# Kernel tuning notes

Measured on AMD Instinct MI355X. Metric: run time of the kernel, lower is better.

The kernel has to match this reference:

```python
import jax, jax.numpy as jnp
import numpy as np

E, K, D = 50000, 8, 256
NH = 4
HD = D // NH
SCALE = HD ** -0.5
EPS = 1e-8


def setup_inputs() -> dict:
    key = jax.random.key(0)
    ks = jax.random.split(key, 16)
    p = lambda k, shp: (jax.random.normal(k, shp, dtype=jnp.float32) * 0.02)
    return {
        "x_i": jax.random.normal(ks[0], (E, D), dtype=jnp.float32),
        "x_j": jax.random.normal(ks[1], (E, D), dtype=jnp.float32),
        "h_seq_i": jax.random.normal(ks[2], (E, K, D), dtype=jnp.float32),
        "h_seq_j": jax.random.normal(ks[3], (E, K, D), dtype=jnp.float32),
        "edge_emb": jax.random.normal(ks[4], (E, D), dtype=jnp.float32),
        "Wq": p(ks[5], (D, D)), "bq": jnp.zeros((D,), jnp.float32),
        "Wk": p(ks[6], (D, D)), "bk": jnp.zeros((D,), jnp.float32),
        "We1": p(ks[7], (D, D // 2)), "be1": jnp.zeros((D // 2,), jnp.float32),
        "We2": p(ks[8], (D // 2, 1)), "be2": jnp.zeros((1,), jnp.float32),
        "Wo1": p(ks[9], (3, 16)), "bo1": jnp.zeros((16,), jnp.float32),
        "Wo2": p(ks[10], (16, 1)), "bo2": jnp.zeros((1,), jnp.float32),
    }


def reference(x_i, x_j, h_seq_i, h_seq_j, edge_emb,
              Wq, bq, Wk, bk, We1, be1, We2, be2, Wo1, bo1, Wo2, bo2):
    # (A) attribute alignment: cosine similarity mapped to (0,1)
    num = jnp.sum(x_i * x_j, axis=-1)
    den = jnp.maximum(jnp.linalg.norm(x_i, axis=-1), EPS) * \
          jnp.maximum(jnp.linalg.norm(x_j, axis=-1), EPS)
    attr_score = (num / den + 1.0) / 2.0  # [E]

    # (B) activity alignment: tiny cross-attention, mean of softmax diagonal
    Q = (jnp.einsum('ekd,df->ekf', h_seq_i, Wq) + bq).reshape(E, K, NH, HD)
    Kv = (jnp.einsum('ekd,df->ekf', h_seq_j, Wk) + bk).reshape(E, K, NH, HD)
    scores = jnp.einsum('eqhd,ekhd->ehqk', Q, Kv) * SCALE  # [E,NH,K,K]
    attn = jax.nn.softmax(scores, axis=-1)
    diag = jnp.diagonal(attn, axis1=-2, axis2=-1)  # [E,NH,K]
    activity_score = diag.mean(axis=(-1, -2))  # [E]

    # (C) edge plausibility MLP (exact GELU as in torch default)
    h = jax.nn.gelu(edge_emb @ We1 + be1, approximate=False)
    edge_score = jax.nn.sigmoid((h @ We2 + be2)[..., 0])  # [E]

    signals = jnp.stack([attr_score, activity_score, edge_score], axis=-1)  # [E,3]
    out = jax.nn.gelu(signals @ Wo1 + bo1, approximate=False) @ Wo2 + bo2
    return jax.nn.sigmoid(out[..., 0])  # [E]
```

## Files before the change

### kernel.cpp

```cpp
#include <hip/hip_runtime.h>

#define E_TOT   50000
#define DD      256
#define KSEQ    8
#define NHEAD   4
#define HDIM    64
#define TE      4
#define SCALE_V 0.125f

typedef __attribute__((ext_vector_type(4))) float f32x4;
typedef __attribute__((ext_vector_type(8))) short short8;

__device__ __forceinline__ unsigned short f2bf(float f) {
    unsigned u = __float_as_uint(f);
    u += 0x7fffu + ((u >> 16) & 1u);
    return (unsigned short)(u >> 16);
}
__device__ __forceinline__ float bf2f(unsigned short h) {
    return __uint_as_float(((unsigned)h) << 16);
}
__device__ __forceinline__ float gelu_exact(float x) {
    return 0.5f * x * (1.0f + erff(x * 0.70710678118654752440f));
}
__device__ __forceinline__ float sigmoidf(float x) {
    return 1.0f / (1.0f + __expf(-x));
}

__global__ void prep_weights(const float* __restrict__ Wq,
                             const float* __restrict__ Wk,
                             const float* __restrict__ We1,
                             unsigned short* __restrict__ wqT,
                             unsigned short* __restrict__ wkT,
                             unsigned short* __restrict__ wb1) {
    int i = blockIdx.x * 256 + threadIdx.x;
    if (i < 131072) {
        int which = i >> 16;
        int j = i & 65535;
        int k = j >> 8, n = j & 255;
        const float* W = which ? Wk : Wq;
        unsigned short* o = which ? wkT : wqT;
        o[n * 256 + k] = f2bf(W[j]);
    } else {
        int j = i - 131072;
        wb1[j] = f2bf(We1[j]);
    }
}

__global__ void score_attr_edge(const float* __restrict__ x_i,
                                const float* __restrict__ x_j,
                                const float* __restrict__ emb,
                                const unsigned short* __restrict__ wb1,
                                const float* __restrict__ be1,
                                const float* __restrict__ We2,
                                const float* __restrict__ be2,
                                float* __restrict__ attr_out,
                                float* __restrict__ edge_out) {
    __shared__ float sEmb[4][DD];
    const int wv = threadIdx.x >> 6;
    const int l  = threadIdx.x & 63;
    const int e  = blockIdx.x * 4 + wv;

    f32x4 a = *(const f32x4*)(x_i + (size_t)e * DD + l * 4);
    f32x4 b = *(const f32x4*)(x_j + (size_t)e * DD + l * 4);
    f32x4 ev = *(const f32x4*)(emb + (size_t)e * DD + l * 4);
    float dot = a[0]*b[0] + a[1]*b[1] + a[2]*b[2] + a[3]*b[3];
    float ni  = a[0]*a[0] + a[1]*a[1] + a[2]*a[2] + a[3]*a[3];
    float nj  = b[0]*b[0] + b[1]*b[1] + b[2]*b[2] + b[3]*b[3];
    #pragma unroll
    for (int off = 1; off < 64; off <<= 1) {
        dot += __shfl_xor(dot, off);
        ni  += __shfl_xor(ni,  off);
        nj  += __shfl_xor(nj,  off);
    }
    float na = fmaxf(sqrtf(ni), 1e-8f);
    float nb = fmaxf(sqrtf(nj), 1e-8f);
    if (l == 0) attr_out[e] = (dot / (na * nb) + 1.0f) * 0.5f;

    sEmb[wv][l*4+0] = ev[0]; sEmb[wv][l*4+1] = ev[1];
    sEmb[wv][l*4+2] = ev[2]; sEmb[wv][l*4+3] = ev[3];
    __syncthreads();

    float acc0 = 0.f, acc1 = 0.f;
    #pragma unroll 8
    for (int k = 0; k < DD; ++k) {
        float ek = sEmb[wv][k];
        unsigned u = *(const unsigned*)(wb1 + k * 128 + 2 * l);
        acc0 = fmaf(ek, bf2f((unsigned short)(u & 0xffffu)), acc0);
        acc1 = fmaf(ek, bf2f((unsigned short)(u >> 16)),     acc1);
    }
    float h0 = gelu_exact(acc0 + be1[2 * l]);
    float h1 = gelu_exact(acc1 + be1[2 * l + 1]);
    float s  = h0 * We2[2 * l] + h1 * We2[2 * l + 1];
    #pragma unroll
    for (int off = 1; off < 64; off <<= 1) s += __shfl_xor(s, off);
    if (l == 0) edge_out[e] = sigmoidf(s + be2[0]);
}

__device__ __forceinline__ void do_gemm(const unsigned short (*A)[DD + 8],
                                        const unsigned short* __restrict__ Wt,
                                        f32x4 acc[2][4], int l, int w) {
    const int lr = l & 15, lq = l >> 4;
    #pragma unroll
    for (int ks = 0; ks < 8; ++ks) {
        const short8 a0 = *(const short8*)&A[lr][ks * 32 + lq * 8];
        const short8 a1 = *(const short8*)&A[16 + lr][ks * 32 + lq * 8];
        #pragma unroll
        for (int n = 0; n < 4; ++n) {
            const int col = (w * 4 + n) * 16 + lr;
            const short8 bv = *(const short8*)(Wt + col * 256 + ks * 32 + lq * 8);
            acc[0][n] = __builtin_amdgcn_mfma_f32_16x16x32_bf16(a0, bv, acc[0][n], 0, 0, 0);
            acc[1][n] = __builtin_amdgcn_mfma_f32_16x16x32_bf16(a1, bv, acc[1][n], 0, 0, 0);
        }
    }
}

__device__ __forceinline__ void writeback(unsigned short (*A)[DD + 8],
                                          const f32x4 acc[2][4],
                                          const float* __restrict__ bias,
                                          int l, int w) {
    const int lr = l & 15, lq = l >> 4;
    #pragma unroll
    for (int n = 0; n < 4; ++n) {
        const int col = (w * 4 + n) * 16 + lr;
        const float bs = bias[col];
        #pragma unroll
        for (int m = 0; m < 2; ++m) {
            #pragma unroll
            for (int v = 0; v < 4; ++v) {
                const int row = m * 16 + lq * 4 + v;
                A[row][col] = f2bf(acc[m][n][v] + bs);
            }
        }
    }
}

__global__ __launch_bounds__(256, 4)
void fused_attn(const float* __restrict__ h_i,
                const float* __restrict__ h_j,
                const unsigned short* __restrict__ wqT,
                const unsigned short* __restrict__ wkT,
                const float* __restrict__ bq,
                const float* __restrict__ bk,
                const float* __restrict__ Wo1,
                const float* __restrict__ bo1,
                const float* __restrict__ Wo2,
                const float* __restrict__ bo2,
                const float* __restrict__ attr_ws,
                const float* __restrict__ edge_ws,
                float* __restrict__ out) {
    __shared__ unsigned short Abf[2][TE * KSEQ][DD + 8];
    __shared__ float actLds[TE];

    const int t = threadIdx.x;
    const int w = t >> 6;
    const int l = t & 63;
    const size_t base = (size_t)blockIdx.x * (TE * KSEQ * DD);

    f32x4 stg[16];
    #pragma unroll
    for (int i = 0; i < 16; ++i) {
        const int f  = i * 256 + t;
        const float* src = (f >> 11) ? h_j : h_i;
        stg[i] = *(const f32x4*)(src + base + (size_t)(f & 2047) * 4);
    }
    #pragma unroll
    for (int i = 0; i < 16; ++i) {
        const int f  = i * 256 + t;
        const int T  = f >> 11;
        const int ff = f & 2047;
        ushort4 u = make_ushort4(f2bf(stg[i][0]), f2bf(stg[i][1]),
                                 f2bf(stg[i][2]), f2bf(stg[i][3]));
        *(ushort4*)&Abf[T][ff >> 6][(ff & 63) * 4] = u;
    }
    __syncthreads();

    {
        f32x4 acc[2][4] = {};
        do_gemm(Abf[0], wqT, acc, l, w);
        __syncthreads();
        writeback(Abf[0], acc, bq, l, w);
    }
    {
        f32x4 acc[2][4] = {};
        do_gemm(Abf[1], wkT, acc, l, w);
        __syncthreads();
        writeback(Abf[1], acc, bk, l, w);
    }
    __syncthreads();

    if (t < 128) {
        const int e = t >> 5, h = (t >> 3) & 3, q = t & 7;
        float qv[64];
        #pragma unroll
        for (int c = 0; c < 8; ++c) {
            short8 v = *(const short8*)&Abf[0][e * 8 + q][h * 64 + c * 8];
            #pragma unroll
            for (int j = 0; j < 8; ++j) qv[c * 8 + j] = bf2f((unsigned short)v[j]);
        }
        float sc[8];
        #pragma unroll
        for (int k = 0; k < 8; ++k) {
            float d = 0.f;
            #pragma unroll
            for (int c = 0; c < 8; ++c) {
                short8 kv = *(const short8*)&Abf[1][e * 8 + k][h * 64 + c * 8];
                #pragma unroll
                for (int j = 0; j < 8; ++j) d = fmaf(qv[c * 8 + j], bf2f((unsigned short)kv[j]), d);
            }
            sc[k] = d * SCALE_V;
        }
        float mx = sc[0];
        #pragma unroll
        for (int k = 1; k < 8; ++k) mx = fmaxf(mx, sc[k]);
        float sum = 0.f, pd = 0.f;
        #pragma unroll
        for (int k = 0; k < 8; ++k) {
            float p = __expf(sc[k] - mx);
            sum += p;
            if (k == q) pd = p;
        }
        float dg = pd / sum;
        #pragma unroll
        for (int off = 1; off < 32; off <<= 1) dg += __shfl_xor(dg, off);
        if ((t & 31) == 0) actLds[e] = dg * (1.0f / 32.0f);
    }
    __syncthreads();

    if (t < TE) {
        const int ge = blockIdx.x * TE + t;
        const float s0 = attr_ws[ge];
        const float s1 = actLds[t];
        const float s2 = edge_ws[ge];
        float acc = bo2[0];
        #pragma unroll
        for (int j = 0; j < 16; ++j) {
            float z = s0 * Wo1[j] + s1 * Wo1[16 + j] + s2 * Wo1[32 + j] + bo1[j];
            acc += gelu_exact(z) * Wo2[j];
        }
        out[ge] = sigmoidf(acc);
    }
}

extern "C" void kernel_launch(void* const* d_in, const int* in_sizes, int n_in,
                              void* d_out, int out_size, void* d_ws, size_t ws_size,
                              hipStream_t stream) {
    const float* x_i  = (const float*)d_in[0];
    const float* x_j  = (const float*)d_in[1];
    const float* h_i  = (const float*)d_in[2];
    const float* h_j  = (const float*)d_in[3];
    const float* emb  = (const float*)d_in[4];
    const float* Wq   = (const float*)d_in[5];
    const float* bq   = (const float*)d_in[6];
    const float* Wk   = (const float*)d_in[7];
    const float* bk   = (const float*)d_in[8];
    const float* We1  = (const float*)d_in[9];
    const float* be1  = (const float*)d_in[10];
    const float* We2  = (const float*)d_in[11];
    const float* be2  = (const float*)d_in[12];
    const float* Wo1  = (const float*)d_in[13];
    const float* bo1  = (const float*)d_in[14];
    const float* Wo2  = (const float*)d_in[15];
    const float* bo2  = (const float*)d_in[16];
    float* out = (float*)d_out;

    unsigned short* wqT = (unsigned short*)d_ws;
    unsigned short* wkT = wqT + 65536;
    unsigned short* wb1 = wkT + 65536;
    float* attr_ws = (float*)((char*)d_ws + 327680);
    float* edge_ws = attr_ws + E_TOT;

    prep_weights<<<640, 256, 0, stream>>>(Wq, Wk, We1, wqT, wkT, wb1);
    score_attr_edge<<<E_TOT / 4, 256, 0, stream>>>(x_i, x_j, emb, wb1, be1, We2, be2,
                                                   attr_ws, edge_ws);
    fused_attn<<<E_TOT / TE, 256, 0, stream>>>(h_i, h_j, wqT, wkT, bq, bk,
                                               Wo1, bo1, Wo2, bo2,
                                               attr_ws, edge_ws, out);
}
```

Baseline: 569.8 us.

## Fuse all score paths into one kernel with LDS DMA and MFMA attention

Merges the attribute/edge scoring kernel into the attention kernel, so one kernel computes cosine, edge MLP, attention and the output MLP without workspace round-trips. h rows are staged through global_load_lds DMA into LDS, with h_j loads overlapped with the Q projection. The edge MLP and the Q·K score computation now use bf16 MFMA instead of scalar FMA loops. LDS use grows and occupancy drops to 3 blocks per CU, and the emb input is rounded to bf16, which changes precision.

```diff
diff --git a/kernel.cpp b/kernel.cpp
--- a/kernel.cpp
+++ b/kernel.cpp
@@ -2,10 +2,8 @@
 
 #define E_TOT   50000
 #define DD      256
-#define KSEQ    8
-#define NHEAD   4
-#define HDIM    64
 #define TE      4
+#define NGROUP  (E_TOT / TE)
 #define SCALE_V 0.125f
 
 typedef __attribute__((ext_vector_type(4))) float f32x4;
@@ -16,14 +14,18 @@
     u += 0x7fffu + ((u >> 16) & 1u);
     return (unsigned short)(u >> 16);
 }
-__device__ __forceinline__ float bf2f(unsigned short h) {
-    return __uint_as_float(((unsigned)h) << 16);
-}
 __device__ __forceinline__ float gelu_exact(float x) {
     return 0.5f * x * (1.0f + erff(x * 0.70710678118654752440f));
 }
 __device__ __forceinline__ float sigmoidf(float x) {
     return 1.0f / (1.0f + __expf(-x));
+}
+
+__device__ __forceinline__ void dma_row16(const float* gbase, float* lds) {
+    const int lane = threadIdx.x & 63;
+    auto gp = (const __attribute__((address_space(1))) char*)(gbase) + lane * 16;
+    auto lp = (__attribute__((address_space(3))) char*)(lds);
+    __builtin_amdgcn_global_load_lds(gp, lp, 16, 0, 0);
 }
 
 __global__ void prep_weights(const float* __restrict__ Wq,
@@ -31,94 +33,43 @@
                              const float* __restrict__ We1,
                              unsigned short* __restrict__ wqT,
                              unsigned short* __restrict__ wkT,
-                             unsigned short* __restrict__ wb1) {
+                             unsigned short* __restrict__ w1T) {
     int i = blockIdx.x * 256 + threadIdx.x;
-    if (i < 131072) {
-        int which = i >> 16;
-        int j = i & 65535;
+    if (i < 65536) {
+        int k = i >> 8, n = i & 255;
+        wqT[n * 256 + k] = f2bf(Wq[i]);
+    } else if (i < 131072) {
+        int j = i - 65536;
         int k = j >> 8, n = j & 255;
-        const float* W = which ? Wk : Wq;
-        unsigned short* o = which ? wkT : wqT;
-        o[n * 256 + k] = f2bf(W[j]);
+        wkT[n * 256 + k] = f2bf(Wk[j]);
     } else {
         int j = i - 131072;
-        wb1[j] = f2bf(We1[j]);
-    }
-}
-
-__global__ void score_attr_edge(const float* __restrict__ x_i,
-                                const float* __restrict__ x_j,
-                                const float* __restrict__ emb,
-                                const unsigned short* __restrict__ wb1,
-                                const float* __restrict__ be1,
-                                const float* __restrict__ We2,
-                                const float* __restrict__ be2,
-                                float* __restrict__ attr_out,
-                                float* __restrict__ edge_out) {
-    __shared__ float sEmb[4][DD];
-    const int wv = threadIdx.x >> 6;
-    const int l  = threadIdx.x & 63;
-    const int e  = blockIdx.x * 4 + wv;
-
-    f32x4 a = *(const f32x4*)(x_i + (size_t)e * DD + l * 4);
-    f32x4 b = *(const f32x4*)(x_j + (size_t)e * DD + l * 4);
-    f32x4 ev = *(const f32x4*)(emb + (size_t)e * DD + l * 4);
-    float dot = a[0]*b[0] + a[1]*b[1] + a[2]*b[2] + a[3]*b[3];
-    float ni  = a[0]*a[0] + a[1]*a[1] + a[2]*a[2] + a[3]*a[3];
-    float nj  = b[0]*b[0] + b[1]*b[1] + b[2]*b[2] + b[3]*b[3];
-    #pragma unroll
-    for (int off = 1; off < 64; off <<= 1) {
-        dot += __shfl_xor(dot, off);
-        ni  += __shfl_xor(ni,  off);
-        nj  += __shfl_xor(nj,  off);
-    }
-    float na = fmaxf(sqrtf(ni), 1e-8f);
-    float nb = fmaxf(sqrtf(nj), 1e-8f);
-    if (l == 0) attr_out[e] = (dot / (na * nb) + 1.0f) * 0.5f;
-
-    sEmb[wv][l*4+0] = ev[0]; sEmb[wv][l*4+1] = ev[1];
-    sEmb[wv][l*4+2] = ev[2]; sEmb[wv][l*4+3] = ev[3];
-    __syncthreads();
-
-    float acc0 = 0.f, acc1 = 0.f;
-    #pragma unroll 8
-    for (int k = 0; k < DD; ++k) {
-        float ek = sEmb[wv][k];
-        unsigned u = *(const unsigned*)(wb1 + k * 128 + 2 * l);
-        acc0 = fmaf(ek, bf2f((unsigned short)(u & 0xffffu)), acc0);
-        acc1 = fmaf(ek, bf2f((unsigned short)(u >> 16)),     acc1);
-    }
-    float h0 = gelu_exact(acc0 + be1[2 * l]);
-    float h1 = gelu_exact(acc1 + be1[2 * l + 1]);
-    float s  = h0 * We2[2 * l] + h1 * We2[2 * l + 1];
-    #pragma unroll
-    for (int off = 1; off < 64; off <<= 1) s += __shfl_xor(s, off);
-    if (l == 0) edge_out[e] = sigmoidf(s + be2[0]);
-}
-
-__device__ __forceinline__ void do_gemm(const unsigned short (*A)[DD + 8],
-                                        const unsigned short* __restrict__ Wt,
-                                        f32x4 acc[2][4], int l, int w) {
-    const int lr = l & 15, lq = l >> 4;
+        int k = j >> 7, n = j & 127;
+        w1T[n * 256 + k] = f2bf(We1[j]);
+    }
+}
+
+__device__ __forceinline__ void proj_gemm(const unsigned short (*A)[260],
+                                          const unsigned short* __restrict__ Wt,
+                                          f32x4 acc[2][4], int lr, int lq, int w) {
     #pragma unroll
     for (int ks = 0; ks < 8; ++ks) {
-        const short8 a0 = *(const short8*)&A[lr][ks * 32 + lq * 8];
-        const short8 a1 = *(const short8*)&A[16 + lr][ks * 32 + lq * 8];
+        short8 a0 = *(const short8*)&A[lr][ks * 32 + lq * 8];
+        short8 a1 = *(const short8*)&A[16 + lr][ks * 32 + lq * 8];
         #pragma unroll
         for (int n = 0; n < 4; ++n) {
             const int col = (w * 4 + n) * 16 + lr;
-            const short8 bv = *(const short8*)(Wt + col * 256 + ks * 32 + lq * 8);
+            short8 bv = *(const short8*)(Wt + col * 256 + ks * 32 + lq * 8);
             acc[0][n] = __builtin_amdgcn_mfma_f32_16x16x32_bf16(a0, bv, acc[0][n], 0, 0, 0);
             acc[1][n] = __builtin_amdgcn_mfma_f32_16x16x32_bf16(a1, bv, acc[1][n], 0, 0, 0);
         }
     }
 }
 
-__device__ __forceinline__ void writeback(unsigned short (*A)[DD + 8],
+__device__ __forceinline__ void writeback(unsigned short (*T)[260],
                                           const f32x4 acc[2][4],
                                           const float* __restrict__ bias,
-                                          int l, int w) {
-    const int lr = l & 15, lq = l >> 4;
+                                          int lr, int lq, int w) {
     #pragma unroll
     for (int n = 0; n < 4; ++n) {
         const int col = (w * 4 + n) * 16 + lr;
@@ -128,117 +79,191 @@
             #pragma unroll
             for (int v = 0; v < 4; ++v) {
                 const int row = m * 16 + lq * 4 + v;
-                A[row][col] = f2bf(acc[m][n][v] + bs);
+                T[row][col] = f2bf(acc[m][n][v] + bs);
             }
         }
     }
 }
 
-__global__ __launch_bounds__(256, 4)
-void fused_attn(const float* __restrict__ h_i,
-                const float* __restrict__ h_j,
-                const unsigned short* __restrict__ wqT,
-                const unsigned short* __restrict__ wkT,
-                const float* __restrict__ bq,
-                const float* __restrict__ bk,
-                const float* __restrict__ Wo1,
-                const float* __restrict__ bo1,
-                const float* __restrict__ Wo2,
-                const float* __restrict__ bo2,
-                const float* __restrict__ attr_ws,
-                const float* __restrict__ edge_ws,
-                float* __restrict__ out) {
-    __shared__ unsigned short Abf[2][TE * KSEQ][DD + 8];
-    __shared__ float actLds[TE];
-
-    const int t = threadIdx.x;
-    const int w = t >> 6;
-    const int l = t & 63;
-    const size_t base = (size_t)blockIdx.x * (TE * KSEQ * DD);
-
-    f32x4 stg[16];
-    #pragma unroll
-    for (int i = 0; i < 16; ++i) {
-        const int f  = i * 256 + t;
-        const float* src = (f >> 11) ? h_j : h_i;
-        stg[i] = *(const f32x4*)(src + base + (size_t)(f & 2047) * 4);
-    }
-    #pragma unroll
-    for (int i = 0; i < 16; ++i) {
-        const int f  = i * 256 + t;
-        const int T  = f >> 11;
-        const int ff = f & 2047;
-        ushort4 u = make_ushort4(f2bf(stg[i][0]), f2bf(stg[i][1]),
-                                 f2bf(stg[i][2]), f2bf(stg[i][3]));
-        *(ushort4*)&Abf[T][ff >> 6][(ff & 63) * 4] = u;
-    }
-    __syncthreads();
-
+__global__ __launch_bounds__(256, 3)
+void fused_all(const float* __restrict__ x_i,
+               const float* __restrict__ x_j,
+               const float* __restrict__ h_i,
+               const float* __restrict__ h_j,
+               const float* __restrict__ emb,
+               const unsigned short* __restrict__ wqT,
+               const unsigned short* __restrict__ wkT,
+               const unsigned short* __restrict__ w1T,
+               const float* __restrict__ bq,
+               const float* __restrict__ bk,
+               const float* __restrict__ be1,
+               const float* __restrict__ We2,
+               const float* __restrict__ be2,
+               const float* __restrict__ Wo1,
+               const float* __restrict__ bo1,
+               const float* __restrict__ Wo2,
+               const float* __restrict__ bo2,
+               float* __restrict__ out) {
+    __shared__ __align__(16) unsigned char ldsA[33280];
+    __shared__ __align__(16) unsigned char ldsH[16640];
+    __shared__ float sEdgeP[4][4];
+
+    float* bufA32 = (float*)ldsA;
+    unsigned short (*bufHI)[260] = (unsigned short (*)[260])ldsH;
+    unsigned short (*tQ)[260]    = (unsigned short (*)[260])ldsA;
+    unsigned short (*tK)[260]    = (unsigned short (*)[260])(ldsA + 16640);
+
+    const int t  = threadIdx.x;
+    const int w  = t >> 6;
+    const int l  = t & 63;
+    const int lr = l & 15, lq = l >> 4;
+    const int g  = blockIdx.x;
+    const size_t rowbase = (size_t)g * 32;
+
+    #pragma unroll
+    for (int rr = 0; rr < 8; ++rr) {
+        const int r = w * 8 + rr;
+        dma_row16(h_i + (rowbase + r) * DD, bufA32 + r * DD);
+    }
+    const int e = g * TE + w;
+    float attr;
     {
-        f32x4 acc[2][4] = {};
-        do_gemm(Abf[0], wqT, acc, l, w);
-        __syncthreads();
-        writeback(Abf[0], acc, bq, l, w);
-    }
+        f32x4 a = *(const f32x4*)(x_i + (size_t)e * DD + l * 4);
+        f32x4 b = *(const f32x4*)(x_j + (size_t)e * DD + l * 4);
+        float dot = a[0]*b[0] + a[1]*b[1] + a[2]*b[2] + a[3]*b[3];
+        float ni  = a[0]*a[0] + a[1]*a[1] + a[2]*a[2] + a[3]*a[3];
+        float nj  = b[0]*b[0] + b[1]*b[1] + b[2]*b[2] + b[3]*b[3];
+        #pragma unroll
+        for (int off = 1; off < 64; off <<= 1) {
+            dot += __shfl_xor(dot, off);
+            ni  += __shfl_xor(ni,  off);
+            nj  += __shfl_xor(nj,  off);
+        }
+        attr = (dot / (fmaxf(sqrtf(ni), 1e-8f) * fmaxf(sqrtf(nj), 1e-8f)) + 1.0f) * 0.5f;
+    }
+    __syncthreads();
+
+    f32x4 stg[8];
+    #pragma unroll
+    for (int i = 0; i < 8; ++i) stg[i] = *(const f32x4*)(bufA32 + (i * 256 + t) * 4);
+    __syncthreads();
+
+    #pragma unroll
+    for (int rr = 0; rr < 8; ++rr) {
+        const int r = w * 8 + rr;
+        dma_row16(h_j + (rowbase + r) * DD, bufA32 + r * DD);
+    }
+    #pragma unroll
+    for (int i = 0; i < 8; ++i) {
+        const int f = i * 256 + t, r = f >> 6, u = f & 63;
+        *(ushort4*)&bufHI[r][u * 4] = make_ushort4(f2bf(stg[i][0]), f2bf(stg[i][1]),
+                                                   f2bf(stg[i][2]), f2bf(stg[i][3]));
+    }
+    __syncthreads();
+
+    f32x4 accQ[2][4] = {};
+    proj_gemm(bufHI, wqT, accQ, lr, lq, w);
+    f32x4 accE[2] = {};
     {
-        f32x4 acc[2][4] = {};
-        do_gemm(Abf[1], wkT, acc, l, w);
-        __syncthreads();
-        writeback(Abf[1], acc, bk, l, w);
-    }
-    __syncthreads();
-
-    if (t < 128) {
-        const int e = t >> 5, h = (t >> 3) & 3, q = t & 7;
-        float qv[64];
-        #pragma unroll
-        for (int c = 0; c < 8; ++c) {
-            short8 v = *(const short8*)&Abf[0][e * 8 + q][h * 64 + c * 8];
+        const float* embrow = emb + ((size_t)g * TE + (lr & 3)) * DD;
+        #pragma unroll
+        for (int ks = 0; ks < 8; ++ks) {
+            f32x4 e0 = *(const f32x4*)(embrow + ks * 32 + lq * 8);
+            f32x4 e1 = *(const f32x4*)(embrow + ks * 32 + lq * 8 + 4);
+            short8 ae;
+            ae[0] = (short)f2bf(e0[0]); ae[1] = (short)f2bf(e0[1]);
+            ae[2] = (short)f2bf(e0[2]); ae[3] = (short)f2bf(e0[3]);
+            ae[4] = (short)f2bf(e1[0]); ae[5] = (short)f2bf(e1[1]);
+            ae[6] = (short)f2bf(e1[2]); ae[7] = (short)f2bf(e1[3]);
             #pragma unroll
-            for (int j = 0; j < 8; ++j) qv[c * 8 + j] = bf2f((unsigned short)v[j]);
-        }
-        float sc[8];
-        #pragma unroll
-        for (int k = 0; k < 8; ++k) {
-            float d = 0.f;
+            for (int n = 0; n < 2; ++n) {
+                const int col = w * 32 + n * 16 + lr;
+                short8 bv = *(const short8*)(w1T + col * 256 + ks * 32 + lq * 8);
+                accE[n] = __builtin_amdgcn_mfma_f32_16x16x32_bf16(ae, bv, accE[n], 0, 0, 0);
+            }
+        }
+    }
+    #pragma unroll
+    for (int i = 0; i < 8; ++i) stg[i] = *(const f32x4*)(bufA32 + (i * 256 + t) * 4);
+    __syncthreads();
+
+    #pragma unroll
+    for (int i = 0; i < 8; ++i) {
+        const int f = i * 256 + t, r = f >> 6, u = f & 63;
+        *(ushort4*)&bufHI[r][u * 4] = make_ushort4(f2bf(stg[i][0]), f2bf(stg[i][1]),
+                                                   f2bf(stg[i][2]), f2bf(stg[i][3]));
+    }
+    writeback(tQ, accQ, bq, lr, lq, w);
+    __syncthreads();
+
+    f32x4 accK[2][4] = {};
+    proj_gemm(bufHI, wkT, accK, lr, lq, w);
+    __syncthreads();
+
+    writeback(tK, accK, bk, lr, lq, w);
+    {
+        float p[4] = {0.f, 0.f, 0.f, 0.f};
+        #pragma unroll
+        for (int n = 0; n < 2; ++n) {
+            const int col = w * 32 + n * 16 + lr;
+            const float b1 = be1[col], w2 = We2[col];
             #pragma unroll
-            for (int c = 0; c < 8; ++c) {
-                short8 kv = *(const short8*)&Abf[1][e * 8 + k][h * 64 + c * 8];
-                #pragma unroll
-                for (int j = 0; j < 8; ++j) d = fmaf(qv[c * 8 + j], bf2f((unsigned short)kv[j]), d);
-            }
-            sc[k] = d * SCALE_V;
-        }
-        float mx = sc[0];
-        #pragma unroll
-        for (int k = 1; k < 8; ++k) mx = fmaxf(mx, sc[k]);
-        float sum = 0.f, pd = 0.f;
-        #pragma unroll
-        for (int k = 0; k < 8; ++k) {
-            float p = __expf(sc[k] - mx);
-            sum += p;
-            if (k == q) pd = p;
-        }
-        float dg = pd / sum;
-        #pragma unroll
-        for (int off = 1; off < 32; off <<= 1) dg += __shfl_xor(dg, off);
-        if ((t & 31) == 0) actLds[e] = dg * (1.0f / 32.0f);
-    }
-    __syncthreads();
-
-    if (t < TE) {
-        const int ge = blockIdx.x * TE + t;
-        const float s0 = attr_ws[ge];
-        const float s1 = actLds[t];
-        const float s2 = edge_ws[ge];
-        float acc = bo2[0];
-        #pragma unroll
-        for (int j = 0; j < 16; ++j) {
-            float z = s0 * Wo1[j] + s1 * Wo1[16 + j] + s2 * Wo1[32 + j] + bo1[j];
-            acc += gelu_exact(z) * Wo2[j];
-        }
-        out[ge] = sigmoidf(acc);
-    }
+            for (int v = 0; v < 4; ++v)
+                p[v] += gelu_exact(accE[n][v] + b1) * w2;
+        }
+        #pragma unroll
+        for (int off = 1; off < 16; off <<= 1) {
+            #pragma unroll
+            for (int v = 0; v < 4; ++v) p[v] += __shfl_xor(p[v], off);
+        }
+        if (l == 0) {
+            sEdgeP[w][0] = p[0]; sEdgeP[w][1] = p[1];
+            sEdgeP[w][2] = p[2]; sEdgeP[w][3] = p[3];
+        }
+    }
+    __syncthreads();
+
+    float contrib = 0.f;
+    #pragma unroll
+    for (int h = 0; h < 4; ++h) {
+        f32x4 s = {};
+        #pragma unroll
+        for (int ks = 0; ks < 2; ++ks) {
+            short8 qa = *(const short8*)&tQ[w * 8 + (lr & 7)][h * 64 + ks * 32 + lq * 8];
+            short8 kb = *(const short8*)&tK[w * 8 + (lr & 7)][h * 64 + ks * 32 + lq * 8];
+            s = __builtin_amdgcn_mfma_f32_16x16x32_bf16(qa, kb, s, 0, 0, 0);
+        }
+        #pragma unroll
+        for (int v = 0; v < 4; ++v) {
+            float sc = s[v] * SCALE_V;
+            float m = sc;
+            m = fmaxf(m, __shfl_xor(m, 1));
+            m = fmaxf(m, __shfl_xor(m, 2));
+            m = fmaxf(m, __shfl_xor(m, 4));
+            float pe = __expf(sc - m);
+            float sum = pe;
+            sum += __shfl_xor(sum, 1);
+            sum += __shfl_xor(sum, 2);
+            sum += __shfl_xor(sum, 4);
+            if (lq < 2 && lr == lq * 4 + v) contrib += pe / sum;
+        }
+    }
+    #pragma unroll
+    for (int off = 1; off < 64; off <<= 1) contrib += __shfl_xor(contrib, off);
+    const float act = contrib * (1.0f / 32.0f);
+
+    const float es = sigmoidf(sEdgeP[0][w] + sEdgeP[1][w] + sEdgeP[2][w] +
+                              sEdgeP[3][w] + be2[0]);
+    float r = 0.f;
+    if (l < 16) {
+        float z = attr * Wo1[l] + act * Wo1[16 + l] + es * Wo1[32 + l] + bo1[l];
+        r = gelu_exact(z) * Wo2[l];
+    }
+    r += __shfl_xor(r, 1);
+    r += __shfl_xor(r, 2);
+    r += __shfl_xor(r, 4);
+    r += __shfl_xor(r, 8);
+    if (l == 0) out[e] = sigmoidf(r + bo2[0]);
 }
 
 extern "C" void kernel_launch(void* const* d_in, const int* in_sizes, int n_in,
@@ -265,14 +290,11 @@
 
     unsigned short* wqT = (unsigned short*)d_ws;
     unsigned short* wkT = wqT + 65536;
-    unsigned short* wb1 = wkT + 65536;
-    float* attr_ws = (float*)((char*)d_ws + 327680);
-    float* edge_ws = attr_ws + E_TOT;
-
-    prep_weights<<<640, 256, 0, stream>>>(Wq, Wk, We1, wqT, wkT, wb1);
-    score_attr_edge<<<E_TOT / 4, 256, 0, stream>>>(x_i, x_j, emb, wb1, be1, We2, be2,
-                                                   attr_ws, edge_ws);
-    fused_attn<<<E_TOT / TE, 256, 0, stream>>>(h_i, h_j, wqT, wkT, bq, bk,
-                                               Wo1, bo1, Wo2, bo2,
-                                               attr_ws, edge_ws, out);
-}
+    unsigned short* w1T = wkT + 65536;
+
+    prep_weights<<<640, 256, 0, stream>>>(Wq, Wk, We1, wqT, wkT, w1T);
+    fused_all<<<NGROUP, 256, 0, stream>>>(x_i, x_j, h_i, h_j, emb,
+                                          wqT, wkT, w1T,
+                                          bq, bk, be1, We2, be2,
+                                          Wo1, bo1, Wo2, bo2, out);
+}
```

Result: slower. 636.1 us (+11.6%).
